# Performance work log

Measured on AMD Instinct MI355X. Metric: run time of the kernel, lower is better.

## Reference

```python
import jax, jax.numpy as jnp
import numpy as np

N = 65536
DIM = 128
MARKET = 32
STYLE = 32
E = 9          # num_market_experts
TOP_K = 3
ALPHA = 1e-4


def setup_inputs() -> dict:
    key = jax.random.key(0)
    ks = jax.random.split(key, 8)
    sc = lambda k, shape, s: (jax.random.normal(k, shape, jnp.float32) * s)
    return {
        "x": jax.random.normal(ks[0], (N, 1, DIM), jnp.float32),
        # Wr: Linear(dim -> market_dim)
        "Wr_w": sc(ks[1], (DIM, MARKET), 0.05),
        "Wr_b": jnp.zeros((MARKET,), jnp.float32),
        # Wl: Linear(N -> 1), applied over the N axis
        "Wl_w": sc(ks[2], (N,), 0.005),
        "Wl_b": jnp.zeros((1,), jnp.float32),
        # router: Linear(dim + market_dim -> E)
        "router_w": sc(ks[3], (DIM + MARKET, E), 0.05),
        "router_b": jnp.zeros((E,), jnp.float32),
        # experts: style params + 2-layer MLP (dim+style -> dim -> dim)
        "styles": sc(ks[4], (E, STYLE), 1.0),
        "W1": sc(ks[5], (E, DIM + STYLE, DIM), 0.05),
        "b1": jnp.zeros((E, DIM), jnp.float32),
        "W2": sc(ks[6], (E, DIM, DIM), 0.05),
        "b2": jnp.zeros((E, DIM), jnp.float32),
    }


def reference(x, Wr_w, Wr_b, Wl_w, Wl_b, router_w, router_b, styles, W1, b1, W2, b2):
    n, s, d = x.shape  # [N, 1, dim]

    # market summary: Wr (relu MLP, dropout=identity in eval), then Wl over N axis
    market = jax.nn.relu(x @ Wr_w + Wr_b)                       # [N,1,M]
    market_g = jnp.einsum('nsm,n->sm', market, Wl_w) + Wl_b     # [1,M]
    market_exp = jnp.broadcast_to(market_g[None], (n, s, market.shape[-1]))
    x_market = jnp.concatenate([x, market_exp], axis=-1)        # [N,1,dim+M]

    # noisy-topk router (noisy=False)
    logits = x_market @ router_w + router_b                     # [N,1,E]
    _top_vals, top_idx = jax.lax.top_k(logits, TOP_K)           # [N,1,K]
    mask = (jax.nn.one_hot(top_idx, E) > 0).any(axis=-2)        # [N,1,E] bool
    sparse = jnp.where(mask, logits, -jnp.inf)
    gating = jax.nn.softmax(sparse, axis=-1)                    # [N,1,E], zeros off top-k

    # sequence-wise auxiliary load-balancing loss
    T = n * s
    flat_g = gating.reshape(-1, E)
    fi = mask.reshape(-1, E).sum(axis=0).astype(jnp.float32) * (E / (TOP_K * T))
    Pi = flat_g.mean(axis=0)
    aux_loss = ALPHA * jnp.sum(fi * Pi)

    # expert MLPs: dense-masked combine (gating is exactly 0 for unselected experts,
    # so this equals the original gather/scatter dispatch)
    flat_x = x.reshape(-1, d)                                   # [T,d]
    W1x = W1[:, :d, :]                                          # [E,d,h]
    W1s = W1[:, d:, :]                                          # [E,style,h]
    style_bias = jnp.einsum('es,esh->eh', styles, W1s) + b1     # [E,h]
    h = jax.nn.relu(jnp.einsum('nd,edh->neh', flat_x, W1x) + style_bias[None])
    out_e = jnp.einsum('neh,ehd->ned', h, W2) + b2[None]        # [T,E,d]
    out = jnp.einsum('ne,ned->nd', flat_g, out_e)               # [T,d]

    return out.reshape(n, s, d), aux_loss
```

## Files before the change

### kernel.cpp

```cpp
#include <hip/hip_runtime.h>
#include <hip/hip_bf16.h>
#include <math.h>

#define NTOK 65536
#define DIM  128
#define NE   9
#define TOPK 3
#define ALPHA_C 1e-4f

using bf16x8 = __attribute__((ext_vector_type(8))) short;
using f32x4  = __attribute__((ext_vector_type(4))) float;

static constexpr size_t OFF_MG   = 0;
static constexpr size_t OFF_CNT  = 128;
static constexpr size_t OFF_GSUM = 192;
static constexpr size_t OFF_SB   = 256;
static constexpr size_t OFF_W1F  = 4864;
static constexpr size_t OFF_W2F  = 299776;

__device__ __forceinline__ unsigned short f2bf(float f) {
    __hip_bfloat16 h = __float2bfloat16(f);
    return *reinterpret_cast<unsigned short*>(&h);
}

__global__ __launch_bounds__(256) void k_prep(const float* __restrict__ x,
    const float* __restrict__ Wrw, const float* __restrict__ Wrb,
    const float* __restrict__ Wlw, float* __restrict__ mg_acc,
    const float* __restrict__ W1, const float* __restrict__ W2,
    unsigned short* __restrict__ W1F, unsigned short* __restrict__ W2F,
    const float* __restrict__ styles, const float* __restrict__ b1,
    float* __restrict__ sb)
{
    __shared__ float smem[64 * 132 + 128 * 32];
    __shared__ float wpart[4][32];
    int bid = blockIdx.x;
    int tid = threadIdx.x;

    if (bid < 1024) {
        float* xs = smem;
        float* wr = smem + 64 * 132;
        int base = bid * 64;
        const float4* x4g = (const float4*)x + (size_t)base * 32;
        for (int i = tid; i < 2048; i += 256) {
            int row = i >> 5, c = i & 31;
            *(float4*)(xs + row * 132 + c * 4) = x4g[i];
        }
        for (int i = tid; i < 1024; i += 256)
            ((float4*)wr)[i] = ((const float4*)Wrw)[i];
        __syncthreads();

        int lane = tid & 63, wv = tid >> 6;
        int tok = wv * 16 + (lane >> 2), sub = lane & 3, m0 = sub * 8;
        float acc[8];
        #pragma unroll
        for (int k = 0; k < 8; ++k) acc[k] = 0.f;
        for (int c = 0; c < 32; ++c) {
            float4 xv = *(const float4*)(xs + tok * 132 + c * 4);
            float xa[4] = {xv.x, xv.y, xv.z, xv.w};
            #pragma unroll
            for (int dd = 0; dd < 4; ++dd)
                #pragma unroll
                for (int k = 0; k < 8; ++k)
                    acc[k] += xa[dd] * wr[(c * 4 + dd) * 32 + m0 + k];
        }
        float wl = Wlw[base + tok];
        #pragma unroll
        for (int k = 0; k < 8; ++k) {
            float v = acc[k] + Wrb[m0 + k];
            acc[k] = (v > 0.f ? v : 0.f) * wl;
        }
        #pragma unroll
        for (int off = 4; off <= 32; off <<= 1)
            #pragma unroll
            for (int k = 0; k < 8; ++k)
                acc[k] += __shfl_xor(acc[k], off);
        if (lane < 4)
            #pragma unroll
            for (int k = 0; k < 8; ++k) wpart[wv][lane * 8 + k] = acc[k];
        __syncthreads();
        if (tid < 32) {
            float s = wpart[0][tid] + wpart[1][tid] + wpart[2][tid] + wpart[3][tid];
            atomicAdd(&mg_acc[tid], s);
        }
    } else if (bid < 1096) {
        int b = bid - 1024;
        int e = b >> 3, n = b & 7;
        int kk = tid >> 6, l = tid & 63;
        int row0 = kk * 32 + (l >> 4) * 8;
        int col  = n * 16 + (l & 15);
        const float* W1e = W1 + (size_t)e * 20480;
        const float* W2e = W2 + (size_t)e * 16384;
        size_t ob = (size_t)e * 16384 + n * 2048 + kk * 512 + l * 8;
        unsigned short u1[8], u2[8];
        #pragma unroll
        for (int j = 0; j < 8; ++j) {
            u1[j] = f2bf(W1e[(size_t)(row0 + j) * 128 + col]);
            u2[j] = f2bf(W2e[(size_t)(row0 + j) * 128 + col]);
        }
        *(ushort4*)(W1F + ob)     = *(ushort4*)(u1);
        *(ushort4*)(W1F + ob + 4) = *(ushort4*)(u1 + 4);
        *(ushort4*)(W2F + ob)     = *(ushort4*)(u2);
        *(ushort4*)(W2F + ob + 4) = *(ushort4*)(u2 + 4);
    } else {
        int e = bid - 1096;
        if (tid < 128) {
            int h = tid;
            float acc = b1[e * 128 + h];
            for (int s = 0; s < 32; ++s)
                acc += styles[e * 32 + s] * W1[(size_t)e * 20480 + (size_t)(128 + s) * 128 + h];
            sb[e * 128 + h] = acc;
        }
    }
}

__global__ void k_aux(const unsigned* __restrict__ cnt, const float* __restrict__ gsum,
                      float* __restrict__ out)
{
    float a = 0.f;
    for (int e = 0; e < 9; ++e) {
        float fi = (float)cnt[e] * ((float)NE / ((float)TOPK * (float)NTOK));
        float Pi = gsum[e] / (float)NTOK;
        a += fi * Pi;
    }
    out[(size_t)NTOK * DIM] = ALPHA_C * a;
}

__global__ __launch_bounds__(256) void k_fused(const float* __restrict__ x,
    const float* __restrict__ rweights, const float* __restrict__ rb,
    const float* __restrict__ mg, const float* __restrict__ Wlb,
    const unsigned short* __restrict__ W1F, const unsigned short* __restrict__ W2F,
    const float* __restrict__ sbg, const float* __restrict__ b2g,
    unsigned* __restrict__ cnt, float* __restrict__ gsum,
    float* __restrict__ out)
{
    __shared__ unsigned short xs[64 * 128];
    __shared__ unsigned short hs[64 * 128];
    __shared__ float garr[64][12];
    __shared__ float ce[9];
    __shared__ unsigned lcount[9];
    __shared__ float lgsum[9];

    float* part = (float*)hs;
    float* rwp  = (float*)hs + 2304;

    int tid = threadIdx.x;
    int base = blockIdx.x * 64;

    for (int i = tid; i < 160 * 9; i += 256) rwp[i] = rweights[i];
    if (tid < 9) { lcount[tid] = 0u; lgsum[tid] = 0.f; }
    __syncthreads();

    int tok = tid >> 2, sub = tid & 3;
    {
        float acc[9];
        #pragma unroll
        for (int e = 0; e < 9; ++e) acc[e] = 0.f;
        const float* xrow = x + (size_t)(base + tok) * 128 + sub;
        for (int d = 0; d < 32; ++d) {
            float xv = xrow[d * 4];
            #pragma unroll
            for (int e = 0; e < 9; ++e) acc[e] += xv * rwp[(d * 4 + sub) * 9 + e];
        }
        #pragma unroll
        for (int e = 0; e < 9; ++e) part[(tok * 4 + sub) * 9 + e] = acc[e];
    }
    if (tid < 9) {
        float c = rb[tid];
        float wlb = Wlb[0];
        for (int m = 0; m < 32; ++m) c += (mg[m] + wlb) * rwp[(128 + m) * 9 + tid];
        ce[tid] = c;
    }
    {
        const float4* x4 = (const float4*)x;
        for (int i = tid; i < 64 * 32; i += 256) {
            int row = i >> 5, p = i & 31;
            float4 v = x4[(size_t)(base + row) * 32 + p];
            unsigned short u[4] = { f2bf(v.x), f2bf(v.y), f2bf(v.z), f2bf(v.w) };
            int sw = ((((p >> 1) ^ (row & 7)) << 4) | ((p & 1) << 3));
            *(ushort4*)((char*)xs + row * 256 + sw) = *(ushort4*)u;
        }
    }
    __syncthreads();

    if (sub == 0) {
        float lg[9];
        #pragma unroll
        for (int e = 0; e < 9; ++e)
            lg[e] = ce[e] + part[(tok * 4 + 0) * 9 + e] + part[(tok * 4 + 1) * 9 + e]
                  + part[(tok * 4 + 2) * 9 + e] + part[(tok * 4 + 3) * 9 + e];
        int used = 0;
        int bi[3]; float bv[3];
        for (int k = 0; k < 3; ++k) {
            float best = -1e30f; int b = -1;
            for (int e = 0; e < 9; ++e)
                if (!((used >> e) & 1) && lg[e] > best) { best = lg[e]; b = e; }
            bi[k] = b; bv[k] = best; used |= 1 << b;
        }
        float p3[3]; float s = 0.f;
        for (int k = 0; k < 3; ++k) { p3[k] = expf(bv[k] - bv[0]); s += p3[k]; }
        #pragma unroll
        for (int e = 0; e < 12; ++e) garr[tok][e] = 0.f;
        for (int k = 0; k < 3; ++k) {
            float g = p3[k] / s;
            garr[tok][bi[k]] = g;
            atomicAdd(&lcount[bi[k]], 1u);
            atomicAdd(&lgsum[bi[k]], g);
        }
    }
    __syncthreads();
    if (tid < 9) {
        atomicAdd(&cnt[tid], lcount[tid]);
        atomicAdd(&gsum[tid], lgsum[tid]);
    }

    int lane = tid & 63, w = tid >> 6;
    int tl = lane & 15;
    int hq = lane >> 4;
    int xr = tl & 7;

    f32x4 acc_out[2][4];
    #pragma unroll
    for (int mi = 0; mi < 2; ++mi)
        #pragma unroll
        for (int ni = 0; ni < 4; ++ni) acc_out[mi][ni] = (f32x4){0.f, 0.f, 0.f, 0.f};

    #pragma unroll 1
    for (int e = 0; e < 9; ++e) {
        const unsigned short* A1 = W1F + (size_t)e * 16384 + (w * 2) * 2048 + lane * 8;
        const unsigned short* A2 = W2F + (size_t)e * 16384 + (w * 2) * 2048 + lane * 8;

        bf16x8 a1[2][4];
        #pragma unroll
        for (int mi = 0; mi < 2; ++mi)
            #pragma unroll
            for (int kk = 0; kk < 4; ++kk)
                a1[mi][kk] = *(const bf16x8*)(A1 + mi * 2048 + kk * 512);

        float4 sbv0 = *(const float4*)(sbg + e * 128 + (w * 2 + 0) * 16 + hq * 4);
        float4 sbv1 = *(const float4*)(sbg + e * 128 + (w * 2 + 1) * 16 + hq * 4);
        f32x4 acc1[2][4];
        #pragma unroll
        for (int ni = 0; ni < 4; ++ni) {
            acc1[0][ni] = (f32x4){sbv0.x, sbv0.y, sbv0.z, sbv0.w};
            acc1[1][ni] = (f32x4){sbv1.x, sbv1.y, sbv1.z, sbv1.w};
        }

        #pragma unroll
        for (int kk = 0; kk < 4; ++kk) {
            #pragma unroll
            for (int ni = 0; ni < 4; ++ni) {
                bf16x8 b = *(const bf16x8*)((const char*)xs + (ni * 16 + tl) * 256
                               + ((((kk * 4 + hq) ^ xr) << 4)));
                acc1[0][ni] = __builtin_amdgcn_mfma_f32_16x16x32_bf16(a1[0][kk], b, acc1[0][ni], 0, 0, 0);
                acc1[1][ni] = __builtin_amdgcn_mfma_f32_16x16x32_bf16(a1[1][kk], b, acc1[1][ni], 0, 0, 0);
            }
        }

        bf16x8 a2[2][4];
        #pragma unroll
        for (int mi = 0; mi < 2; ++mi)
            #pragma unroll
            for (int kk = 0; kk < 4; ++kk)
                a2[mi][kk] = *(const bf16x8*)(A2 + mi * 2048 + kk * 512);

        #pragma unroll
        for (int ni = 0; ni < 4; ++ni) {
            int t = ni * 16 + tl;
            float g = garr[t][e];
            char* rowp = (char*)hs + t * 256;
            #pragma unroll
            for (int mi = 0; mi < 2; ++mi) {
                f32x4 v = acc1[mi][ni];
                unsigned short u[4];
                u[0] = f2bf(fmaxf(v[0], 0.f) * g);
                u[1] = f2bf(fmaxf(v[1], 0.f) * g);
                u[2] = f2bf(fmaxf(v[2], 0.f) * g);
                u[3] = f2bf(fmaxf(v[3], 0.f) * g);
                int chunk = (w * 2 + mi) * 2 + (hq >> 1);
                int off = (hq & 1) * 8;
                *(ushort4*)(rowp + (((chunk ^ xr) << 4) | off)) = *(ushort4*)u;
            }
        }
        __syncthreads();

        #pragma unroll
        for (int kk = 0; kk < 4; ++kk) {
            #pragma unroll
            for (int ni = 0; ni < 4; ++ni) {
                bf16x8 b = *(const bf16x8*)((const char*)hs + (ni * 16 + tl) * 256
                               + ((((kk * 4 + hq) ^ xr) << 4)));
                acc_out[0][ni] = __builtin_amdgcn_mfma_f32_16x16x32_bf16(a2[0][kk], b, acc_out[0][ni], 0, 0, 0);
                acc_out[1][ni] = __builtin_amdgcn_mfma_f32_16x16x32_bf16(a2[1][kk], b, acc_out[1][ni], 0, 0, 0);
            }
        }
        if (e != 8) __syncthreads();
    }

    #pragma unroll
    for (int mi = 0; mi < 2; ++mi) {
        int d0 = (w * 2 + mi) * 16 + hq * 4;
        float4 b2v[9];
        #pragma unroll
        for (int e = 0; e < 9; ++e) b2v[e] = *(const float4*)(b2g + e * 128 + d0);
        #pragma unroll
        for (int ni = 0; ni < 4; ++ni) {
            int t = ni * 16 + tl;
            float4 bias = {0.f, 0.f, 0.f, 0.f};
            #pragma unroll
            for (int e = 0; e < 9; ++e) {
                float g = garr[t][e];
                bias.x += g * b2v[e].x; bias.y += g * b2v[e].y;
                bias.z += g * b2v[e].z; bias.w += g * b2v[e].w;
            }
            f32x4 v = acc_out[mi][ni];
            float4 r = {v[0] + bias.x, v[1] + bias.y, v[2] + bias.z, v[3] + bias.w};
            *(float4*)(out + (size_t)(base + t) * 128 + d0) = r;
        }
    }
}

extern "C" void kernel_launch(void* const* d_in, const int* in_sizes, int n_in,
                              void* d_out, int out_size, void* d_ws, size_t ws_size,
                              hipStream_t stream) {
    const float* x      = (const float*)d_in[0];
    const float* Wrw    = (const float*)d_in[1];
    const float* Wrb    = (const float*)d_in[2];
    const float* Wlw    = (const float*)d_in[3];
    const float* Wlb    = (const float*)d_in[4];
    const float* rw     = (const float*)d_in[5];
    const float* rb     = (const float*)d_in[6];
    const float* styles = (const float*)d_in[7];
    const float* W1     = (const float*)d_in[8];
    const float* b1     = (const float*)d_in[9];
    const float* W2     = (const float*)d_in[10];
    const float* b2     = (const float*)d_in[11];
    float* out = (float*)d_out;

    char* ws = (char*)d_ws;
    float*          mg    = (float*)(ws + OFF_MG);
    unsigned*       cnt   = (unsigned*)(ws + OFF_CNT);
    float*          gsum  = (float*)(ws + OFF_GSUM);
    float*          sbp   = (float*)(ws + OFF_SB);
    unsigned short* W1F   = (unsigned short*)(ws + OFF_W1F);
    unsigned short* W2F   = (unsigned short*)(ws + OFF_W2F);

    hipMemsetAsync(ws, 0, 256, stream);

    k_prep<<<1105, 256, 0, stream>>>(x, Wrw, Wrb, Wlw, mg, W1, W2, W1F, W2F,
                                     styles, b1, sbp);
    k_fused<<<1024, 256, 0, stream>>>(x, rw, rb, mg, Wlb, W1F, W2F, sbp, b2,
                                      cnt, gsum, out);
    k_aux<<<1, 1, 0, stream>>>(cnt, gsum, out);
}
```

Measured before the change: 190.9 us.

## Restructure market projection per-token and prefetch next expert W1 fragments

Result: no change. 194.5 us (+1.9%).

```diff
diff --git a/kernel.cpp b/kernel.cpp
--- a/kernel.cpp
+++ b/kernel.cpp
@@ -31,59 +31,69 @@
     const float* __restrict__ styles, const float* __restrict__ b1,
     float* __restrict__ sb)
 {
-    __shared__ float smem[64 * 132 + 128 * 32];
+    __shared__ float xs[256 * 132];
     __shared__ float wpart[4][32];
     int bid = blockIdx.x;
     int tid = threadIdx.x;
 
-    if (bid < 1024) {
-        float* xs = smem;
-        float* wr = smem + 64 * 132;
-        int base = bid * 64;
+    if (bid < 256) {
+        int base = bid * 256;
         const float4* x4g = (const float4*)x + (size_t)base * 32;
-        for (int i = tid; i < 2048; i += 256) {
+        for (int i = tid; i < 256 * 32; i += 256) {
             int row = i >> 5, c = i & 31;
             *(float4*)(xs + row * 132 + c * 4) = x4g[i];
         }
-        for (int i = tid; i < 1024; i += 256)
-            ((float4*)wr)[i] = ((const float4*)Wrw)[i];
         __syncthreads();
 
-        int lane = tid & 63, wv = tid >> 6;
-        int tok = wv * 16 + (lane >> 2), sub = lane & 3, m0 = sub * 8;
-        float acc[8];
-        #pragma unroll
-        for (int k = 0; k < 8; ++k) acc[k] = 0.f;
+        float acc[32];
+        #pragma unroll
+        for (int m = 0; m < 32; ++m) acc[m] = 0.f;
+
+        const float* xrow = xs + tid * 132;
         for (int c = 0; c < 32; ++c) {
-            float4 xv = *(const float4*)(xs + tok * 132 + c * 4);
+            float4 xv = *(const float4*)(xrow + c * 4);
             float xa[4] = {xv.x, xv.y, xv.z, xv.w};
             #pragma unroll
-            for (int dd = 0; dd < 4; ++dd)
+            for (int dd = 0; dd < 4; ++dd) {
+                int d = c * 4 + dd;
                 #pragma unroll
-                for (int k = 0; k < 8; ++k)
-                    acc[k] += xa[dd] * wr[(c * 4 + dd) * 32 + m0 + k];
-        }
-        float wl = Wlw[base + tok];
-        #pragma unroll
-        for (int k = 0; k < 8; ++k) {
-            float v = acc[k] + Wrb[m0 + k];
-            acc[k] = (v > 0.f ? v : 0.f) * wl;
-        }
-        #pragma unroll
-        for (int off = 4; off <= 32; off <<= 1)
-            #pragma unroll
-            for (int k = 0; k < 8; ++k)
-                acc[k] += __shfl_xor(acc[k], off);
-        if (lane < 4)
-            #pragma unroll
-            for (int k = 0; k < 8; ++k) wpart[wv][lane * 8 + k] = acc[k];
+                for (int mq = 0; mq < 8; ++mq) {
+                    float4 wv = *(const float4*)(Wrw + d * 32 + mq * 4);
+                    acc[mq * 4 + 0] += xa[dd] * wv.x;
+                    acc[mq * 4 + 1] += xa[dd] * wv.y;
+                    acc[mq * 4 + 2] += xa[dd] * wv.z;
+                    acc[mq * 4 + 3] += xa[dd] * wv.w;
+                }
+            }
+        }
+
+        float wl = Wlw[base + tid];
+        #pragma unroll
+        for (int mq = 0; mq < 8; ++mq) {
+            float4 bv = *(const float4*)(Wrb + mq * 4);
+            float ba[4] = {bv.x, bv.y, bv.z, bv.w};
+            #pragma unroll
+            for (int j = 0; j < 4; ++j) {
+                float v = acc[mq * 4 + j] + ba[j];
+                acc[mq * 4 + j] = (v > 0.f ? v : 0.f) * wl;
+            }
+        }
+        #pragma unroll
+        for (int off = 1; off <= 32; off <<= 1)
+            #pragma unroll
+            for (int m = 0; m < 32; ++m)
+                acc[m] += __shfl_xor(acc[m], off);
+        int lane = tid & 63, wv_ = tid >> 6;
+        if (lane == 0)
+            #pragma unroll
+            for (int m = 0; m < 32; ++m) wpart[wv_][m] = acc[m];
         __syncthreads();
         if (tid < 32) {
             float s = wpart[0][tid] + wpart[1][tid] + wpart[2][tid] + wpart[3][tid];
             atomicAdd(&mg_acc[tid], s);
         }
-    } else if (bid < 1096) {
-        int b = bid - 1024;
+    } else if (bid < 328) {
+        int b = bid - 256;
         int e = b >> 3, n = b & 7;
         int kk = tid >> 6, l = tid & 63;
         int row0 = kk * 32 + (l >> 4) * 8;
@@ -102,7 +112,7 @@
         *(ushort4*)(W2F + ob)     = *(ushort4*)(u2);
         *(ushort4*)(W2F + ob + 4) = *(ushort4*)(u2 + 4);
     } else {
-        int e = bid - 1096;
+        int e = bid - 328;
         if (tid < 128) {
             int h = tid;
             float acc = b1[e * 128 + h];
@@ -224,18 +234,18 @@
         #pragma unroll
         for (int ni = 0; ni < 4; ++ni) acc_out[mi][ni] = (f32x4){0.f, 0.f, 0.f, 0.f};
 
+    const unsigned short* A1b = W1F + (w * 2) * 2048 + lane * 8;
+    const unsigned short* A2b = W2F + (w * 2) * 2048 + lane * 8;
+
+    bf16x8 a1c[2][4];
+    #pragma unroll
+    for (int mi = 0; mi < 2; ++mi)
+        #pragma unroll
+        for (int kk = 0; kk < 4; ++kk)
+            a1c[mi][kk] = *(const bf16x8*)(A1b + mi * 2048 + kk * 512);
+
     #pragma unroll 1
     for (int e = 0; e < 9; ++e) {
-        const unsigned short* A1 = W1F + (size_t)e * 16384 + (w * 2) * 2048 + lane * 8;
-        const unsigned short* A2 = W2F + (size_t)e * 16384 + (w * 2) * 2048 + lane * 8;
-
-        bf16x8 a1[2][4];
-        #pragma unroll
-        for (int mi = 0; mi < 2; ++mi)
-            #pragma unroll
-            for (int kk = 0; kk < 4; ++kk)
-                a1[mi][kk] = *(const bf16x8*)(A1 + mi * 2048 + kk * 512);
-
         float4 sbv0 = *(const float4*)(sbg + e * 128 + (w * 2 + 0) * 16 + hq * 4);
         float4 sbv1 = *(const float4*)(sbg + e * 128 + (w * 2 + 1) * 16 + hq * 4);
         f32x4 acc1[2][4];
@@ -245,23 +255,25 @@
             acc1[1][ni] = (f32x4){sbv1.x, sbv1.y, sbv1.z, sbv1.w};
         }
 
+        __builtin_amdgcn_s_setprio(1);
         #pragma unroll
         for (int kk = 0; kk < 4; ++kk) {
             #pragma unroll
             for (int ni = 0; ni < 4; ++ni) {
                 bf16x8 b = *(const bf16x8*)((const char*)xs + (ni * 16 + tl) * 256
                                + ((((kk * 4 + hq) ^ xr) << 4)));
-                acc1[0][ni] = __builtin_amdgcn_mfma_f32_16x16x32_bf16(a1[0][kk], b, acc1[0][ni], 0, 0, 0);
-                acc1[1][ni] = __builtin_amdgcn_mfma_f32_16x16x32_bf16(a1[1][kk], b, acc1[1][ni], 0, 0, 0);
-            }
-        }
+                acc1[0][ni] = __builtin_amdgcn_mfma_f32_16x16x32_bf16(a1c[0][kk], b, acc1[0][ni], 0, 0, 0);
+                acc1[1][ni] = __builtin_amdgcn_mfma_f32_16x16x32_bf16(a1c[1][kk], b, acc1[1][ni], 0, 0, 0);
+            }
+        }
+        __builtin_amdgcn_s_setprio(0);
 
         bf16x8 a2[2][4];
         #pragma unroll
         for (int mi = 0; mi < 2; ++mi)
             #pragma unroll
             for (int kk = 0; kk < 4; ++kk)
-                a2[mi][kk] = *(const bf16x8*)(A2 + mi * 2048 + kk * 512);
+                a2[mi][kk] = *(const bf16x8*)(A2b + (size_t)e * 16384 + mi * 2048 + kk * 512);
 
         #pragma unroll
         for (int ni = 0; ni < 4; ++ni) {
@@ -281,8 +293,16 @@
                 *(ushort4*)(rowp + (((chunk ^ xr) << 4) | off)) = *(ushort4*)u;
             }
         }
+        if (e != 8) {
+            #pragma unroll
+            for (int mi = 0; mi < 2; ++mi)
+                #pragma unroll
+                for (int kk = 0; kk < 4; ++kk)
+                    a1c[mi][kk] = *(const bf16x8*)(A1b + (size_t)(e + 1) * 16384 + mi * 2048 + kk * 512);
+        }
         __syncthreads();
 
+        __builtin_amdgcn_s_setprio(1);
         #pragma unroll
         for (int kk = 0; kk < 4; ++kk) {
             #pragma unroll
@@ -293,6 +313,7 @@
                 acc_out[1][ni] = __builtin_amdgcn_mfma_f32_16x16x32_bf16(a2[1][kk], b, acc_out[1][ni], 0, 0, 0);
             }
         }
+        __builtin_amdgcn_s_setprio(0);
         if (e != 8) __syncthreads();
     }
 
@@ -346,8 +367,8 @@
 
     hipMemsetAsync(ws, 0, 256, stream);
 
-    k_prep<<<1105, 256, 0, stream>>>(x, Wrw, Wrb, Wlw, mg, W1, W2, W1F, W2F,
-                                     styles, b1, sbp);
+    k_prep<<<337, 256, 0, stream>>>(x, Wrw, Wrb, Wlw, mg, W1, W2, W1F, W2F,
+                                    styles, b1, sbp);
     k_fused<<<1024, 256, 0, stream>>>(x, rw, rb, mg, Wlb, W1F, W2F, sbp, b2,
                                       cnt, gsum, out);
     k_aux<<<1, 1, 0, stream>>>(cnt, gsum, out);
```
